# Optimization experiments

Measured on AMD Instinct MI355X. Metric: run time of the kernel, lower is better.

## Reference

```python
import jax, jax.numpy as jnp
import numpy as np

B, T, C = 4, 512, 1024          # batch, seq, n_embd
E, H = 8, 2048                  # n_total_experts, ffn hidden (ffn_factor*C)
N_SHARED, K = 1, 2              # shared experts, top-k routed
ROUTE_SCALE = 1.0


def setup_inputs() -> dict:
    key = jax.random.key(0)
    ks = jax.random.split(key, 6)
    s = 0.02
    return {
        "x": jax.random.normal(ks[0], (B, T, C), jnp.float32),
        "gate_w": jax.random.normal(ks[1], (C, E), jnp.float32) * s,
        "gate_b": jnp.zeros((E,), jnp.float32),
        "w1": jax.random.normal(ks[2], (E, C, H), jnp.float32) * s,
        "b1": jnp.zeros((E, H), jnp.float32),
        "w2": jax.random.normal(ks[3], (E, H, C), jnp.float32) * s,
        "b2": jnp.zeros((E, C), jnp.float32),
        "w3": jax.random.normal(ks[4], (E, C, H), jnp.float32) * s,
        "b3": jnp.zeros((E, H), jnp.float32),
    }


def reference(x, gate_w, gate_b, w1, b1, w2, b2, w3, b3):
    Bs, Ts, Cs = x.shape
    N = Bs * Ts
    xf = x.reshape(N, Cs)

    # --- gating (softmax in fp32, as in the torch code) ---
    logits = xf @ gate_w + gate_b                       # [N, E]
    scores = jax.nn.softmax(logits.astype(jnp.float32), axis=-1).astype(logits.dtype)

    topk_vals, topk_idx = jax.lax.top_k(scores[:, N_SHARED:], K)   # routed experts
    shared_ix = jnp.broadcast_to(jnp.arange(N_SHARED), (N, N_SHARED))
    all_idx = jnp.concatenate([shared_ix, topk_idx + N_SHARED], axis=-1)  # [N, S+K]
    all_w = jnp.concatenate([scores[:, :N_SHARED], topk_vals], axis=-1) * ROUTE_SCALE

    # combine-weight matrix: each expert selected at most once per token
    rows = jnp.arange(N)[:, None]
    cw = jnp.zeros((N, E), x.dtype).at[rows, all_idx].add(all_w)  # [N, E]

    # --- per-expert SwiGLU MLP (vectorized over experts; zero cw masks out) ---
    a = jnp.einsum('nc,ech->neh', xf, w1) + b1          # [N, E, H]
    g = jnp.einsum('nc,ech->neh', xf, w3) + b3
    h = jax.nn.silu(g) * a
    out = jnp.einsum('neh,ehc,ne->nc', h, w2, cw) + cw @ b2  # weighted combine

    # --- balance loss ---
    flat_idx = all_idx.reshape(-1)
    usage = jnp.zeros((E,), jnp.float32).at[flat_idx].add(1.0)
    score_sum = jnp.zeros((E,), jnp.float32).at[flat_idx].add(all_w.reshape(-1).astype(jnp.float32))
    Kp = float(N_SHARED + K)
    bal_loss = jnp.sum((float(E) / (Kp * N)) * usage * (score_sum / N))

    return out.reshape(Bs, Ts, Cs), bal_loss
```

## Files before the change

### kernel.cpp

```cpp
#include <hip/hip_runtime.h>
#include <stdint.h>

#define N_TOK 2048
#define C_DIM 1024
#define H_DIM 2048
#define NE 8
#define NSLOT 3

#define BM 128
#define BN 128
#define BK 64
#define PGRID 1024

#define WS_COUNTS   0
#define WS_PLAN     256
#define WS_CW       (WS_PLAN + 1024)
#define WS_ROUTE    (WS_CW + N_TOK*NE*4)
#define WS_LISTS    (WS_ROUTE + N_TOK*4)
#define WS_XB       (WS_LISTS + NE*N_TOK*4)
#define WS_HBUF     (WS_XB + (size_t)N_TOK*C_DIM*2)
#define WS_OUTSLOT  (WS_HBUF + (size_t)N_TOK*NSLOT*H_DIM*2)
#define WS_WT1T     (WS_OUTSLOT + (size_t)N_TOK*NSLOT*C_DIM*2)
#define WS_WT3T     (WS_WT1T + (size_t)NE*H_DIM*C_DIM*2)
#define WS_WT2T     (WS_WT3T + (size_t)NE*H_DIM*C_DIM*2)

typedef short bf16x8 __attribute__((ext_vector_type(8)));
typedef float f32x4 __attribute__((ext_vector_type(4)));

union FragU { bf16x8 v; uint2 u2[2]; };

__device__ __forceinline__ unsigned short f2b(float f) {
    union { float f; uint32_t u; } v; v.f = f;
    return (unsigned short)((v.u + 0x7fffu + ((v.u >> 16) & 1u)) >> 16);
}
__device__ __forceinline__ float b2f(unsigned short s) {
    union { uint32_t u; float f; } v; v.u = ((uint32_t)s) << 16; return v.f;
}

__device__ __forceinline__ void gload16(const unsigned short* g, unsigned short* l) {
    __builtin_amdgcn_global_load_lds(
        (const __attribute__((address_space(1))) unsigned int*)g,
        (__attribute__((address_space(3))) unsigned int*)l, 16, 0, 0);
}

__device__ __forceinline__ void tcast256(
        const float* __restrict__ src, unsigned short* __restrict__ dtile0,
        int N, int NKT, int kt, int nBase, char* lb, int t) {
    uint32_t* L = (uint32_t*)lb;
    const int l = t & 63, w = t >> 6;
    const float* s = src + (size_t)(kt * 64) * N + nBase;
#pragma unroll 4
    for (int i = 0; i < 16; i++) {
        int k = w * 16 + i;
        float4 v = *(const float4*)(s + (size_t)k * N + 4 * l);
        uint2 p;
        p.x = (uint32_t)f2b(v.x) | ((uint32_t)f2b(v.y) << 16);
        p.y = (uint32_t)f2b(v.z) | ((uint32_t)f2b(v.w) << 16);
        *(uint2*)(L + k * 130 + 2 * l) = p;
    }
    __syncthreads();
    const int rn = t >> 3, cc = t & 7;
#pragma unroll
    for (int s2 = 0; s2 < 8; s2++) {
        int n = s2 * 32 + rn;
        int np = n >> 1, hi = (n & 1) * 16;
        uint32_t o[4];
#pragma unroll
        for (int u = 0; u < 4; u++) {
            uint32_t a = L[(cc * 8 + 2 * u) * 130 + np];
            uint32_t b = L[(cc * 8 + 2 * u + 1) * 130 + np];
            o[u] = ((a >> hi) & 0xffffu) | (((b >> hi) & 0xffffu) << 16);
        }
        unsigned short* drow = dtile0 + (size_t)s2 * NKT * 2048 + rn * 64 + cc * 8;
        *(uint4*)drow = *(uint4*)o;
    }
}

__global__ __launch_bounds__(256) void prep_kernel(
        const float* __restrict__ x, const float* __restrict__ gw,
        const float* __restrict__ gb, const float* __restrict__ w1,
        const float* __restrict__ w3, float* __restrict__ cw,
        unsigned short* __restrict__ xb, int* __restrict__ route,
        unsigned short* __restrict__ wt1t, unsigned short* __restrict__ wt3t) {
    __shared__ __align__(16) char smem[33792];
    const int b = blockIdx.x;
    if (b >= 512) {
        int bb = b - 512;
        int op = bb >> 10, r2 = bb & 1023;
        int e = r2 >> 7, rem = r2 & 127, kt = rem >> 3, nB = rem & 7;
        const float* src = (op ? w3 : w1) + (size_t)e * C_DIM * H_DIM;
        unsigned short* dst = (op ? wt3t : wt1t) +
                              ((size_t)(e * 64 + nB * 8) * 16 + kt) * 2048;
        tcast256(src, dst, H_DIM, 16, kt, nB * 256, smem, threadIdx.x);
        return;
    }
    int n = (b * 256 + threadIdx.x) >> 6;
    int lane = threadIdx.x & 63;
    float acc[NE];
#pragma unroll
    for (int e = 0; e < NE; e++) acc[e] = 0.f;
    for (int c = lane; c < C_DIM; c += 64) {
        float xv = x[n * C_DIM + c];
        xb[n * C_DIM + c] = f2b(xv);
        const float* g = gw + c * NE;
#pragma unroll
        for (int e = 0; e < NE; e++) acc[e] += xv * g[e];
    }
#pragma unroll
    for (int e = 0; e < NE; e++) {
#pragma unroll
        for (int off = 32; off >= 1; off >>= 1) acc[e] += __shfl_xor(acc[e], off, 64);
        acc[e] += gb[e];
    }
    float m = acc[0];
#pragma unroll
    for (int e = 1; e < NE; e++) m = fmaxf(m, acc[e]);
    float s = 0.f, sc[NE];
#pragma unroll
    for (int e = 0; e < NE; e++) { sc[e] = __expf(acc[e] - m); s += sc[e]; }
    float inv = 1.f / s;
#pragma unroll
    for (int e = 0; e < NE; e++) sc[e] *= inv;
    int i1 = 1; float v1 = sc[1];
#pragma unroll
    for (int e = 2; e < NE; e++) if (sc[e] > v1) { v1 = sc[e]; i1 = e; }
    int i2 = 0; float v2 = -1.f;
#pragma unroll
    for (int e = 1; e < NE; e++) if (e != i1 && sc[e] > v2) { v2 = sc[e]; i2 = e; }
    if (lane < NE) {
        float v = 0.f;
        if (lane == 0) v = sc[0];
        else if (lane == i1) v = v1;
        else if (lane == i2) v = v2;
        cw[n * NE + lane] = v;
    }
    if (lane == 0) route[n] = i1 | (i2 << 8);
}

__global__ void lists_kernel(const int* __restrict__ route, int* __restrict__ counts,
                             int* __restrict__ lists) {
    const int e = blockIdx.x, lane = threadIdx.x;
    if (e == 0) {
        for (int base = 0; base < N_TOK; base += 64)
            lists[base + lane] = (base + lane) * 4;
        if (lane == 0) counts[0] = N_TOK;
        return;
    }
    int cnt = 0;
    for (int base = 0; base < N_TOK; base += 64) {
        int r = route[base + lane];
        int i1 = r & 255, i2 = (r >> 8) & 255;
        bool mt = (i1 == e) || (i2 == e);
        int slot = (i1 == e) ? 1 : 2;
        unsigned long long mask = __ballot(mt);
        int pos = __popcll(mask & ((1ull << lane) - 1ull));
        if (mt) lists[e * N_TOK + cnt + pos] = (base + lane) * 4 + slot;
        cnt += __popcll(mask);
    }
    if (lane == 0) counts[e] = cnt;
}

__global__ void plan_kernel(const int* __restrict__ counts, int* __restrict__ plan) {
    if (threadIdx.x == 0) {
        int p = 0;
        for (int e = 0; e < NE; e++) {
            int nb = (counts[e] + BM - 1) / BM;
            for (int m = 0; m < nb; m++) plan[1 + p++] = (e << 8) | m;
        }
        plan[0] = p;
    }
}

#define STAGE(NA, NB, aoff, boff) do {                                    \
    _Pragma("unroll")                                                     \
    for (int i_ = 0; i_ < (NA); i_++)                                     \
        gload16(asrc[i_] + (aoff), As + (i_ * 256 + t) * 8);              \
    _Pragma("unroll")                                                     \
    for (int i_ = 0; i_ < (NB); i_++)                                     \
        gload16(bsrc[i_] + (boff), Bs + (i_ * 256 + t) * 8);              \
} while (0)

#define COMPUTE(NT, BEXPR) do {                                           \
    __builtin_amdgcn_s_setprio(1);                                        \
    _Pragma("unroll")                                                     \
    for (int j_ = 0; j_ < 2; j_++) {                                      \
        FragU af[4], bf[NT];                                              \
        _Pragma("unroll")                                                 \
        for (int mt = 0; mt < 4; mt++) {                                  \
            int row = wr * 64 + mt * 16 + ln15;                           \
            int slot = (j_ * 4 + lg) ^ swz;                               \
            af[mt].v = *(const bf16x8*)(As + row * BK + slot * 8);        \
        }                                                                 \
        _Pragma("unroll")                                                 \
        for (int nt = 0; nt < (NT); nt++) {                               \
            int row = (BEXPR);                                            \
            int slot = (j_ * 4 + lg) ^ swz;                               \
            bf[nt].v = *(const bf16x8*)(Bs + row * BK + slot * 8);        \
        }                                                                 \
        _Pragma("unroll")                                                 \
        for (int mt = 0; mt < 4; mt++)                                    \
            _Pragma("unroll")                                             \
            for (int nt = 0; nt < (NT); nt++)                             \
                acc[mt][nt] = __builtin_amdgcn_mfma_f32_16x16x32_bf16(    \
                    af[mt].v, bf[nt].v, acc[mt][nt], 0, 0, 0);            \
    }                                                                     \
    __builtin_amdgcn_s_setprio(0);                                        \
} while (0)

#define KLOOP(NK, NA, NB, NT, BEXPR) do {                                 \
    for (int kt = 0; kt < (NK); kt++) {                                   \
        STAGE(NA, NB, kt * BK, kt * 2048);                                \
        asm volatile("s_waitcnt vmcnt(0)" ::: "memory");                  \
        __builtin_amdgcn_s_barrier();                                     \
        COMPUTE(NT, BEXPR);                                               \
        __builtin_amdgcn_s_barrier();                                     \
    }                                                                     \
} while (0)

__global__ __launch_bounds__(256, 4) void expert_up_kernel(
        const unsigned short* __restrict__ xb, const unsigned short* __restrict__ wt1t,
        const unsigned short* __restrict__ wt3t, const float* __restrict__ b1,
        const float* __restrict__ b3, const int* __restrict__ counts,
        const int* __restrict__ lists, const int* __restrict__ plan,
        unsigned short* __restrict__ hbuf, const float* __restrict__ w2,
        unsigned short* __restrict__ wt2t) {
    const int t = threadIdx.x;
    const int lane = t & 63, w = t >> 6;
    const int ln15 = lane & 15, lg = lane >> 4;
    const int wr = w >> 1, wc = w & 1;
    const int swz = ln15 & 7;

    __shared__ __align__(16) char smem[33792];
    unsigned short* As = (unsigned short*)smem;
    unsigned short* Bs = (unsigned short*)(smem + BM * BK * 2);
    int* rowtok = (int*)(smem + BM * BK * 2 + BN * BK * 2);

    const int ntile = plan[0] << 5;
    for (int tile = blockIdx.x; tile < ntile; tile += PGRID) {
        const int mi = tile >> 5, nb = tile & 31;
        const int ent = plan[1 + mi];
        const int e = ent >> 8, m0 = (ent & 255) * BM;
        const int cnt = counts[e];

        if (t < BM) {
            int r = m0 + t;
            rowtok[t] = lists[e * N_TOK + (r < cnt ? r : cnt - 1)];
        }
        __syncthreads();

        const unsigned short* asrc[4];
        const unsigned short* bsrc[4];
#pragma unroll
        for (int i = 0; i < 4; i++) {
            int c = i * 256 + t;
            int row = c >> 3, kc = (c & 7) ^ (row & 7);
            asrc[i] = xb + (size_t)(rowtok[row] >> 2) * C_DIM + kc * 8;
        }
#pragma unroll
        for (int i = 0; i < 4; i++) {
            int c = i * 256 + t;
            int r = c >> 3, kc = (c & 7) ^ (r & 7);
            int g = r >> 4;
            const unsigned short* wb = (g & 1) ? wt3t : wt1t;
            int rb = nb * 2 + (g >> 2);
            int trow = ((g >> 1) & 1) * 16 + (r & 15);
            bsrc[i] = wb + ((size_t)(e * 64 + rb) * 16) * 2048 + trow * 64 + kc * 8;
        }

        f32x4 acc[4][4];
#pragma unroll
        for (int a = 0; a < 4; a++)
#pragma unroll
            for (int b = 0; b < 4; b++) acc[a][b] = (f32x4){0.f, 0.f, 0.f, 0.f};

        KLOOP(C_DIM / BK, 4, 4, 4, wc * 64 + nt * 16 + ln15);

#pragma unroll
        for (int p = 0; p < 2; p++) {
            int h = nb * 64 + (wc * 2 + p) * 16 + ln15;
            float bb1 = b1[e * H_DIM + h], bb3 = b3[e * H_DIM + h];
#pragma unroll
            for (int mt = 0; mt < 4; mt++) {
#pragma unroll
                for (int jj = 0; jj < 4; jj++) {
                    int mrow = wr * 64 + mt * 16 + lg * 4 + jj;
                    float av = acc[mt][2 * p][jj] + bb1;
                    float gv = acc[mt][2 * p + 1][jj] + bb3;
                    float hv = av * gv / (1.f + __expf(-gv));
                    int ent2 = rowtok[mrow];
                    hbuf[(size_t)((ent2 >> 2) * NSLOT + (ent2 & 3)) * H_DIM + h] = f2b(hv);
                }
            }
        }
        __syncthreads();
    }

    {
        int bb = blockIdx.x;
        int e = bb >> 7, rem = bb & 127, kt = rem >> 2, nB = rem & 3;
        tcast256(w2 + (size_t)e * H_DIM * C_DIM,
                 wt2t + ((size_t)(e * 32 + nB * 8) * 32 + kt) * 2048,
                 C_DIM, 32, kt, nB * 256, smem, t);
    }
}

__global__ __launch_bounds__(256, 4) void expert_down_kernel(
        const unsigned short* __restrict__ hbuf, const unsigned short* __restrict__ wt2t,
        const float* __restrict__ b2, const float* __restrict__ cw,
        const int* __restrict__ counts, const int* __restrict__ lists,
        const int* __restrict__ plan, unsigned short* __restrict__ outslot) {
    const int t = threadIdx.x;
    const int lane = t & 63, w = t >> 6;
    const int ln15 = lane & 15, lg = lane >> 4;
    const int wr = w >> 1, wc = w & 1;
    const int swz = ln15 & 7;

    __shared__ __align__(16) unsigned short As[BM * BK];
    __shared__ __align__(16) unsigned short Bs[64 * BK];
    __shared__ int rowtok[BM];

    const int ntile = plan[0] << 4;
    for (int tile = blockIdx.x; tile < ntile; tile += PGRID) {
        const int mi = tile >> 4, nb = tile & 15;
        const int ent = plan[1 + mi];
        const int e = ent >> 8, m0 = (ent & 255) * BM;
        const int cnt = counts[e];
        const int c0 = nb * 64;

        if (t < BM) {
            int r = m0 + t;
            rowtok[t] = lists[e * N_TOK + (r < cnt ? r : cnt - 1)];
        }
        __syncthreads();

        const unsigned short* asrc[4];
        const unsigned short* bsrc[2];
#pragma unroll
        for (int i = 0; i < 4; i++) {
            int c = i * 256 + t;
            int row = c >> 3, kc = (c & 7) ^ (row & 7);
            int ent2 = rowtok[row];
            asrc[i] = hbuf + (size_t)((ent2 >> 2) * NSLOT + (ent2 & 3)) * H_DIM + kc * 8;
        }
#pragma unroll
        for (int i = 0; i < 2; i++) {
            int c = i * 256 + t;
            int row = c >> 3, kc = (c & 7) ^ (row & 7);
            bsrc[i] = wt2t + (size_t)(e * 32 + nb * 2 + (row >> 5)) * 32 * 2048 +
                      (size_t)(row & 31) * 64 + kc * 8;
        }

        f32x4 acc[4][2];
#pragma unroll
        for (int a = 0; a < 4; a++)
#pragma unroll
            for (int b = 0; b < 2; b++) acc[a][b] = (f32x4){0.f, 0.f, 0.f, 0.f};

        KLOOP(H_DIM / BK, 4, 2, 2, wc * 32 + nt * 16 + ln15);

#pragma unroll
        for (int nt = 0; nt < 2; nt++) {
            int col = c0 + wc * 32 + nt * 16 + ln15;
            float bb = b2[e * C_DIM + col];
#pragma unroll
            for (int mt = 0; mt < 4; mt++) {
#pragma unroll
                for (int jj = 0; jj < 4; jj++) {
                    int mrow = wr * 64 + mt * 16 + lg * 4 + jj;
                    int ent2 = rowtok[mrow];
                    int tok = ent2 >> 2, slot = ent2 & 3;
                    float cwv = cw[tok * NE + e];
                    outslot[(size_t)(tok * NSLOT + slot) * C_DIM + col] =
                        f2b(cwv * (acc[mt][nt][jj] + bb));
                }
            }
        }
        __syncthreads();
    }
}

__global__ __launch_bounds__(256) void reduce_loss_kernel(
        const unsigned short* __restrict__ os, const float* __restrict__ cw,
        const int* __restrict__ counts, float* __restrict__ out) {
    if (blockIdx.x < 1024) {
        int i = blockIdx.x * 256 + threadIdx.x;
        int n = i >> 7;
        int c = (i & 127) * 8;
        const unsigned short* p0 = os + ((size_t)n * NSLOT + 0) * C_DIM + c;
        const unsigned short* p1 = os + ((size_t)n * NSLOT + 1) * C_DIM + c;
        const unsigned short* p2 = os + ((size_t)n * NSLOT + 2) * C_DIM + c;
        uint4 a = *(const uint4*)p0, b = *(const uint4*)p1, d = *(const uint4*)p2;
        const unsigned short* sa = (const unsigned short*)&a;
        const unsigned short* sb = (const unsigned short*)&b;
        const unsigned short* sd = (const unsigned short*)&d;
        float r[8];
#pragma unroll
        for (int j = 0; j < 8; j++) r[j] = b2f(sa[j]) + b2f(sb[j]) + b2f(sd[j]);
        float* o = out + (size_t)n * C_DIM + c;
        *(float4*)o = *(float4*)&r[0];
        *(float4*)(o + 4) = *(float4*)&r[4];
    } else if (threadIdx.x < 64) {
        int lane = threadIdx.x;
        float ss[NE];
#pragma unroll
        for (int e = 0; e < NE; e++) ss[e] = 0.f;
        for (int n = lane; n < N_TOK; n += 64) {
#pragma unroll
            for (int e = 0; e < NE; e++) ss[e] += cw[n * NE + e];
        }
#pragma unroll
        for (int e = 0; e < NE; e++) {
#pragma unroll
            for (int off = 32; off >= 1; off >>= 1) ss[e] += __shfl_xor(ss[e], off, 64);
        }
        if (lane == 0) {
            float bal = 0.f;
            const float fac = (float)NE / (3.f * (float)N_TOK * (float)N_TOK);
#pragma unroll
            for (int e = 0; e < NE; e++) bal += fac * (float)counts[e] * ss[e];
            out[(size_t)N_TOK * C_DIM] = bal;
        }
    }
}

extern "C" void kernel_launch(void* const* d_in, const int* in_sizes, int n_in,
                              void* d_out, int out_size, void* d_ws, size_t ws_size,
                              hipStream_t stream) {
    const float* x  = (const float*)d_in[0];
    const float* gw = (const float*)d_in[1];
    const float* gb = (const float*)d_in[2];
    const float* w1 = (const float*)d_in[3];
    const float* b1 = (const float*)d_in[4];
    const float* w2 = (const float*)d_in[5];
    const float* b2 = (const float*)d_in[6];
    const float* w3 = (const float*)d_in[7];
    const float* b3 = (const float*)d_in[8];
    float* out = (float*)d_out;
    char* ws = (char*)d_ws;
    int*            counts = (int*)(ws + WS_COUNTS);
    int*            plan   = (int*)(ws + WS_PLAN);
    float*          cw     = (float*)(ws + WS_CW);
    int*            route  = (int*)(ws + WS_ROUTE);
    int*            lists  = (int*)(ws + WS_LISTS);
    unsigned short* xb     = (unsigned short*)(ws + WS_XB);
    unsigned short* hbuf   = (unsigned short*)(ws + WS_HBUF);
    unsigned short* oslot  = (unsigned short*)(ws + WS_OUTSLOT);
    unsigned short* wt1t   = (unsigned short*)(ws + WS_WT1T);
    unsigned short* wt3t   = (unsigned short*)(ws + WS_WT3T);
    unsigned short* wt2t   = (unsigned short*)(ws + WS_WT2T);

    hipLaunchKernelGGL(prep_kernel, dim3(2560), dim3(256), 0, stream,
                       x, gw, gb, w1, w3, cw, xb, route, wt1t, wt3t);
    hipLaunchKernelGGL(lists_kernel, dim3(NE), dim3(64), 0, stream,
                       route, counts, lists);
    hipLaunchKernelGGL(plan_kernel, dim3(1), dim3(64), 0, stream, counts, plan);
    hipLaunchKernelGGL(expert_up_kernel, dim3(PGRID), dim3(256), 0, stream,
                       xb, wt1t, wt3t, b1, b3, counts, lists, plan, hbuf, w2, wt2t);
    hipLaunchKernelGGL(expert_down_kernel, dim3(PGRID), dim3(256), 0, stream,
                       hbuf, wt2t, b2, cw, counts, lists, plan, oslot);
    hipLaunchKernelGGL(reduce_loss_kernel, dim3(1025), dim3(256), 0, stream,
                       oslot, cw, counts, out);
}
```

Measured before the change: 196.3 us.

## Double-buffer LDS tiles so global loads overlap MFMA compute in expert GEMMs

Replaces the single-buffer K loop in the expert up and down GEMMs with a ping-pong scheme. The next K tile is staged into a second LDS buffer while MFMAs consume the current one, leaving one barrier per tile instead of two and hiding global load latency. LDS per block roughly doubles, and launch bounds drop from 4 to 2 (up) and 3 (down) blocks per CU, trading occupancy for overlap. The w2 transpose tail in the up kernel still uses the shared smem buffer.

```diff
diff --git a/kernel.cpp b/kernel.cpp
--- a/kernel.cpp
+++ b/kernel.cpp
@@ -171,16 +171,16 @@
     }
 }
 
-#define STAGE(NA, NB, aoff, boff) do {                                    \
+#define STAGE(A_, B_, NA, NB, aoff, boff) do {                            \
     _Pragma("unroll")                                                     \
     for (int i_ = 0; i_ < (NA); i_++)                                     \
-        gload16(asrc[i_] + (aoff), As + (i_ * 256 + t) * 8);              \
+        gload16(asrc[i_] + (aoff), (A_) + (i_ * 256 + t) * 8);            \
     _Pragma("unroll")                                                     \
     for (int i_ = 0; i_ < (NB); i_++)                                     \
-        gload16(bsrc[i_] + (boff), Bs + (i_ * 256 + t) * 8);              \
+        gload16(bsrc[i_] + (boff), (B_) + (i_ * 256 + t) * 8);            \
 } while (0)
 
-#define COMPUTE(NT, BEXPR) do {                                           \
+#define COMPUTE(A_, B_, NT, BEXPR) do {                                   \
     __builtin_amdgcn_s_setprio(1);                                        \
     _Pragma("unroll")                                                     \
     for (int j_ = 0; j_ < 2; j_++) {                                      \
@@ -189,13 +189,13 @@
         for (int mt = 0; mt < 4; mt++) {                                  \
             int row = wr * 64 + mt * 16 + ln15;                           \
             int slot = (j_ * 4 + lg) ^ swz;                               \
-            af[mt].v = *(const bf16x8*)(As + row * BK + slot * 8);        \
+            af[mt].v = *(const bf16x8*)((A_) + row * BK + slot * 8);      \
         }                                                                 \
         _Pragma("unroll")                                                 \
         for (int nt = 0; nt < (NT); nt++) {                               \
             int row = (BEXPR);                                            \
             int slot = (j_ * 4 + lg) ^ swz;                               \
-            bf[nt].v = *(const bf16x8*)(Bs + row * BK + slot * 8);        \
+            bf[nt].v = *(const bf16x8*)((B_) + row * BK + slot * 8);      \
         }                                                                 \
         _Pragma("unroll")                                                 \
         for (int mt = 0; mt < 4; mt++)                                    \
@@ -207,17 +207,24 @@
     __builtin_amdgcn_s_setprio(0);                                        \
 } while (0)
 
-#define KLOOP(NK, NA, NB, NT, BEXPR) do {                                 \
-    for (int kt = 0; kt < (NK); kt++) {                                   \
-        STAGE(NA, NB, kt * BK, kt * 2048);                                \
+#define KLOOP2(NK, NA, NB, NT, BEXPR) do {                                \
+    STAGE(As0_, Bs0_, NA, NB, 0, 0);                                      \
+    asm volatile("s_waitcnt vmcnt(0)" ::: "memory");                      \
+    __builtin_amdgcn_s_barrier();                                         \
+    for (int kt = 0; kt < (NK); kt += 2) {                                \
+        STAGE(As1_, Bs1_, NA, NB, (kt + 1) * BK, (kt + 1) * 2048);        \
+        COMPUTE(As0_, Bs0_, NT, BEXPR);                                   \
         asm volatile("s_waitcnt vmcnt(0)" ::: "memory");                  \
         __builtin_amdgcn_s_barrier();                                     \
-        COMPUTE(NT, BEXPR);                                               \
+        if (kt + 2 < (NK))                                                \
+            STAGE(As0_, Bs0_, NA, NB, (kt + 2) * BK, (kt + 2) * 2048);    \
+        COMPUTE(As1_, Bs1_, NT, BEXPR);                                   \
+        asm volatile("s_waitcnt vmcnt(0)" ::: "memory");                  \
         __builtin_amdgcn_s_barrier();                                     \
     }                                                                     \
 } while (0)
 
-__global__ __launch_bounds__(256, 4) void expert_up_kernel(
+__global__ __launch_bounds__(256, 2) void expert_up_kernel(
         const unsigned short* __restrict__ xb, const unsigned short* __restrict__ wt1t,
         const unsigned short* __restrict__ wt3t, const float* __restrict__ b1,
         const float* __restrict__ b3, const int* __restrict__ counts,
@@ -230,10 +237,12 @@
     const int wr = w >> 1, wc = w & 1;
     const int swz = ln15 & 7;
 
-    __shared__ __align__(16) char smem[33792];
-    unsigned short* As = (unsigned short*)smem;
-    unsigned short* Bs = (unsigned short*)(smem + BM * BK * 2);
-    int* rowtok = (int*)(smem + BM * BK * 2 + BN * BK * 2);
+    __shared__ __align__(16) char smem[66048];
+    unsigned short* As0_ = (unsigned short*)smem;
+    unsigned short* As1_ = (unsigned short*)(smem + 16384);
+    unsigned short* Bs0_ = (unsigned short*)(smem + 32768);
+    unsigned short* Bs1_ = (unsigned short*)(smem + 49152);
+    int* rowtok = (int*)(smem + 65536);
 
     const int ntile = plan[0] << 5;
     for (int tile = blockIdx.x; tile < ntile; tile += PGRID) {
@@ -273,7 +282,7 @@
 #pragma unroll
             for (int b = 0; b < 4; b++) acc[a][b] = (f32x4){0.f, 0.f, 0.f, 0.f};
 
-        KLOOP(C_DIM / BK, 4, 4, 4, wc * 64 + nt * 16 + ln15);
+        KLOOP2(C_DIM / BK, 4, 4, 4, wc * 64 + nt * 16 + ln15);
 
 #pragma unroll
         for (int p = 0; p < 2; p++) {
@@ -304,7 +313,7 @@
     }
 }
 
-__global__ __launch_bounds__(256, 4) void expert_down_kernel(
+__global__ __launch_bounds__(256, 3) void expert_down_kernel(
         const unsigned short* __restrict__ hbuf, const unsigned short* __restrict__ wt2t,
         const float* __restrict__ b2, const float* __restrict__ cw,
         const int* __restrict__ counts, const int* __restrict__ lists,
@@ -315,9 +324,12 @@
     const int wr = w >> 1, wc = w & 1;
     const int swz = ln15 & 7;
 
-    __shared__ __align__(16) unsigned short As[BM * BK];
-    __shared__ __align__(16) unsigned short Bs[64 * BK];
-    __shared__ int rowtok[BM];
+    __shared__ __align__(16) char smem[49664];
+    unsigned short* As0_ = (unsigned short*)smem;
+    unsigned short* As1_ = (unsigned short*)(smem + 16384);
+    unsigned short* Bs0_ = (unsigned short*)(smem + 32768);
+    unsigned short* Bs1_ = (unsigned short*)(smem + 40960);
+    int* rowtok = (int*)(smem + 49152);
 
     const int ntile = plan[0] << 4;
     for (int tile = blockIdx.x; tile < ntile; tile += PGRID) {
@@ -356,7 +368,7 @@
 #pragma unroll
             for (int b = 0; b < 2; b++) acc[a][b] = (f32x4){0.f, 0.f, 0.f, 0.f};
 
-        KLOOP(H_DIM / BK, 4, 2, 2, wc * 32 + nt * 16 + ln15);
+        KLOOP2(H_DIM / BK, 4, 2, 2, wc * 32 + nt * 16 + ln15);
 
 #pragma unroll
         for (int nt = 0; nt < 2; nt++) {
```

After: 200.2 us. About the same (+2.0%).
